# Performance work log

Measured on AMD Instinct MI355X. Metric: run time of the kernel, lower is better.

Reference implementation:

```python
import jax, jax.numpy as jnp
import numpy as np

N_NODES = 40000
N_EDGES = 640000
D = 128
N_GRAPHS = 64


def gcn_conv(x, W, b, edge_index):
    """PyG-style GCNConv: add self-loops, symmetric norm, linear, scatter-add."""
    n = x.shape[0]
    loops = jnp.arange(n, dtype=edge_index.dtype)
    src = jnp.concatenate([edge_index[0], loops])  # message sources (x_j)
    dst = jnp.concatenate([edge_index[1], loops])  # aggregation targets
    # deg computed over targets (col) with unit edge weights, incl. self-loops
    deg = jax.ops.segment_sum(jnp.ones_like(src, dtype=x.dtype), dst, num_segments=n)
    dinv = jnp.where(deg > 0, jax.lax.rsqrt(jnp.maximum(deg, 1.0)), 0.0)
    norm = dinv[src] * dinv[dst]  # [E+N]
    h = x @ W  # [N, d_out]
    out = jax.ops.segment_sum(norm[:, None] * h[src], dst, num_segments=n)
    return out + b


def global_mean_pool(x, batch, num_graphs):
    summed = jax.ops.segment_sum(x, batch, num_segments=num_graphs)
    counts = jax.ops.segment_sum(jnp.ones((x.shape[0],), x.dtype), batch, num_segments=num_graphs)
    return summed / jnp.maximum(counts, 1.0)[:, None]


def setup_inputs() -> dict:
    key = jax.random.key(0)
    ks = jax.random.split(key, 6)
    x = jax.random.normal(ks[0], (N_NODES, D), dtype=jnp.float32)
    edge_index = jax.random.randint(ks[1], (2, N_EDGES), 0, N_NODES)
    batch = jnp.sort(jax.random.randint(ks[2], (N_NODES,), 0, N_GRAPHS))
    s = 1.0 / np.sqrt(D)
    W1 = jax.random.normal(ks[3], (D, D), dtype=jnp.float32) * s
    W2 = jax.random.normal(ks[4], (D, D), dtype=jnp.float32) * s
    b1 = jnp.zeros((D,), jnp.float32)
    b2 = jnp.zeros((D,), jnp.float32)
    return {"x": x, "edge_index": edge_index, "batch": batch,
            "W1": W1, "b1": b1, "W2": W2, "b2": b2}


def reference(x, edge_index, batch, W1, b1, W2, b2):
    h = jax.nn.relu(gcn_conv(x, W1, b1, edge_index))
    h = gcn_conv(h, W2, b2, edge_index)  # no ReLU on last layer
    return global_mean_pool(h, batch, N_GRAPHS)
```

## Files before the change

### kernel.cpp

```cpp
#include <hip/hip_runtime.h>

#define D 128
#define N_GRAPHS 64

typedef unsigned int uint32;
typedef __attribute__((ext_vector_type(8))) _Float16 f16x8;
typedef __attribute__((ext_vector_type(4))) float f32x4;

__device__ __forceinline__ float hl(uint32 u) {
    return (float)__builtin_bit_cast(_Float16, (unsigned short)(u & 0xFFFF));
}
__device__ __forceinline__ float hh(uint32 u) {
    return (float)__builtin_bit_cast(_Float16, (unsigned short)(u >> 16));
}
__device__ __forceinline__ uint32 h2pair(float a, float b) {
    unsigned short ua = __builtin_bit_cast(unsigned short, (_Float16)a);
    unsigned short ub = __builtin_bit_cast(unsigned short, (_Float16)b);
    return (uint32)ua | ((uint32)ub << 16);
}

__global__ __launch_bounds__(256) void prep_kernel(int* __restrict__ cnt,
                                                   const float* __restrict__ W1,
                                                   uint32* __restrict__ Wh, int n) {
    int i = blockIdx.x * 256 + threadIdx.x;
    if (i < n) {
        cnt[i] = 0;
    } else if (i < n + D * (D / 2)) {
        int j = i - n;
        int nn = j & 127, kd = j >> 7;
        float v0 = W1[(size_t)(2 * kd) * D + nn];
        float v1 = W1[(size_t)(2 * kd + 1) * D + nn];
        Wh[nn * 64 + kd] = h2pair(v0, v1);
    }
}


__global__ void count_rank_kernel(const int* __restrict__ dst, int* __restrict__ cnt,
                                  int* __restrict__ rank, int E) {
    int e = blockIdx.x * blockDim.x + threadIdx.x;
    if (e < E) rank[e] = atomicAdd(&cnt[dst[e]], 1);
}

__global__ __launch_bounds__(1024) void scanA_kernel(const int* __restrict__ cnt,
                                                     int* __restrict__ rowptr,
                                                     int* __restrict__ tot,
                                                     float* __restrict__ dinv,
                                                     float* __restrict__ c,
                                                     const int* __restrict__ batch, int n) {
    __shared__ int swave[16];
    int t = threadIdx.x;
    int lane = t & 63, wave = t >> 6;
    int i = blockIdx.x * 1024 + t;
    {
        size_t f4base = (size_t)blockIdx.x * 1024 * 16;
        size_t f4lim = (size_t)n * 16;
        float4 z = make_float4(0.f, 0.f, 0.f, 0.f);
#pragma unroll
        for (int q = 0; q < 16; ++q) {
            size_t idx = f4base + (size_t)q * 1024 + t;
            if (idx < f4lim) ((float4*)c)[idx] = z;
        }
    }
    int orig = (i < n) ? cnt[i] : 0;
    int v = orig;
#pragma unroll
    for (int off = 1; off < 64; off <<= 1) {
        int u = __shfl_up(v, off, 64);
        if (lane >= off) v += u;
    }
    if (lane == 63) swave[wave] = v;
    __syncthreads();
    if (wave == 0) {
        int wv = (lane < 16) ? swave[lane] : 0;
#pragma unroll
        for (int off = 1; off < 16; off <<= 1) {
            int u = __shfl_up(wv, off, 64);
            if (lane >= off) wv += u;
        }
        if (lane < 16) swave[lane] = wv;
    }
    if (i < n) {
        float dv = rsqrtf((float)(orig + 1));
        dinv[i] = dv;
        c[(size_t)i * N_GRAPHS + batch[i]] = dv * dv;
    }
    __syncthreads();
    int incl = v + ((wave > 0) ? swave[wave - 1] : 0);
    if (i < n) rowptr[i] = incl - orig;
    if (t == 1023) tot[blockIdx.x] = incl;
}

__global__ __launch_bounds__(1024) void scanB_kernel(int* __restrict__ rowptr,
                                                     const int* __restrict__ tot,
                                                     int n, int nchunks) {
    __shared__ int soff;
    int b = blockIdx.x, t = threadIdx.x;
    if (t == 0) {
        int o = 0;
        for (int j = 0; j < b; ++j) o += tot[j];
        soff = o;
    }
    __syncthreads();
    int i = b * 1024 + t;
    if (i < n) rowptr[i] += soff;
    if (b == 0 && t == 0) {
        int o = 0;
        for (int j = 0; j < nchunks; ++j) o += tot[j];
        rowptr[n] = o;
    }
}


#define GBM 64

__global__ __launch_bounds__(256) void fill_gemm_kernel(
    const float* __restrict__ A, const uint32* __restrict__ Wh,
    uint32* __restrict__ hb, int M, int gemmBlocks,
    const int* __restrict__ src, const int* __restrict__ dst,
    const int* __restrict__ rowptr, const int* __restrict__ rank,
    int* __restrict__ col, const float* __restrict__ dinv,
    float* __restrict__ c, const int* __restrict__ batch, int E) {
    __shared__ uint32 lds[64 * 68];

    if (blockIdx.x >= gemmBlocks) {
        int e = (blockIdx.x - gemmBlocks) * 256 + threadIdx.x;
        if (e < E) {
            int s = src[e], d = dst[e];
            int pos = rowptr[d] + rank[e];
            col[pos] = s;
            float w = dinv[s] * dinv[d];
            atomicAdd(&c[(size_t)s * N_GRAPHS + batch[d]], w);
        }
        return;
    }

    uint32* As = lds;
    int tid = threadIdx.x;
    int row0 = blockIdx.x * GBM;

#pragma unroll
    for (int j = 0; j < 8; ++j) {
        int idx = tid + j * 256;
        int r = idx >> 5, c4 = idx & 31;
        float4 v = make_float4(0.f, 0.f, 0.f, 0.f);
        if (row0 + r < M) v = *(const float4*)&A[(size_t)(row0 + r) * D + c4 * 4];
        As[r * 68 + c4 * 2 + 0] = h2pair(v.x, v.y);
        As[r * 68 + c4 * 2 + 1] = h2pair(v.z, v.w);
    }
    __syncthreads();

    int wave = tid >> 6, lane = tid & 63;
    int quad = lane >> 4, l16 = lane & 15;
    int wr = (wave & 1) * 32;
    int wc = (wave >> 1) * 64;
    f32x4 acc[2][4];
#pragma unroll
    for (int mi = 0; mi < 2; ++mi)
#pragma unroll
        for (int ni = 0; ni < 4; ++ni) acc[mi][ni] = (f32x4){0.f, 0.f, 0.f, 0.f};

#pragma unroll
    for (int ks = 0; ks < 4; ++ks) {
        int kd = ks * 16 + quad * 4;
        f16x8 a0 = *(f16x8*)&As[(wr + l16) * 68 + kd];
        f16x8 a1 = *(f16x8*)&As[(wr + 16 + l16) * 68 + kd];
        f16x8 b0 = *(const f16x8*)&Wh[(wc + l16) * 64 + kd];
        f16x8 b1 = *(const f16x8*)&Wh[(wc + 16 + l16) * 64 + kd];
        f16x8 b2 = *(const f16x8*)&Wh[(wc + 32 + l16) * 64 + kd];
        f16x8 b3 = *(const f16x8*)&Wh[(wc + 48 + l16) * 64 + kd];
        acc[0][0] = __builtin_amdgcn_mfma_f32_16x16x32_f16(a0, b0, acc[0][0], 0, 0, 0);
        acc[0][1] = __builtin_amdgcn_mfma_f32_16x16x32_f16(a0, b1, acc[0][1], 0, 0, 0);
        acc[0][2] = __builtin_amdgcn_mfma_f32_16x16x32_f16(a0, b2, acc[0][2], 0, 0, 0);
        acc[0][3] = __builtin_amdgcn_mfma_f32_16x16x32_f16(a0, b3, acc[0][3], 0, 0, 0);
        acc[1][0] = __builtin_amdgcn_mfma_f32_16x16x32_f16(a1, b0, acc[1][0], 0, 0, 0);
        acc[1][1] = __builtin_amdgcn_mfma_f32_16x16x32_f16(a1, b1, acc[1][1], 0, 0, 0);
        acc[1][2] = __builtin_amdgcn_mfma_f32_16x16x32_f16(a1, b2, acc[1][2], 0, 0, 0);
        acc[1][3] = __builtin_amdgcn_mfma_f32_16x16x32_f16(a1, b3, acc[1][3], 0, 0, 0);
    }
    __syncthreads();

    unsigned short* cs = (unsigned short*)lds;
#pragma unroll
    for (int mi = 0; mi < 2; ++mi)
#pragma unroll
        for (int ni = 0; ni < 4; ++ni)
#pragma unroll
            for (int r = 0; r < 4; ++r) {
                int row = wr + mi * 16 + quad * 4 + r;
                int col2 = wc + ni * 16 + l16;
                cs[row * 128 + col2] =
                    __builtin_bit_cast(unsigned short, (_Float16)acc[mi][ni][r]);
            }
    __syncthreads();
#pragma unroll
    for (int j = 0; j < 4; ++j) {
        int idx = tid + j * 256;
        int r = idx >> 4, q = idx & 15;
        if (row0 + r < M)
            *(uint4*)&hb[(size_t)(row0 + r) * 64 + q * 4] = *(uint4*)&lds[r * 64 + q * 4];
    }
}


__global__ __launch_bounds__(128) void agg_kernel(const uint32* __restrict__ hb,
                                                  const int* __restrict__ rowptr,
                                                  const int* __restrict__ col,
                                                  const float* __restrict__ dinv,
                                                  const float* __restrict__ bias,
                                                  uint32* __restrict__ h1, int n) {
    int tid = threadIdx.x;
    int lane32 = tid & 31;
    int slot = tid >> 5;
    int node = blockIdx.x * 4 + slot;
    if (node >= n) return;
    const uint2* __restrict__ h2 = (const uint2*)hb;

    float di = dinv[node];
    float ws = di * di;
    uint2 su = h2[(size_t)node * 32 + lane32];
    float a0 = ws * hl(su.x), a1 = ws * hh(su.x);
    float a2 = ws * hl(su.y), a3 = ws * hh(su.y);

    int k = rowptr[node], end = rowptr[node + 1];
    for (; k + 8 <= end; k += 8) {
        uint2 v[8];
        float w[8];
#pragma unroll
        for (int j = 0; j < 8; ++j) {
            int s = col[k + j];
            w[j] = dinv[s] * di;
            v[j] = h2[(size_t)s * 32 + lane32];
        }
#pragma unroll
        for (int j = 0; j < 8; ++j) {
            a0 = fmaf(w[j], hl(v[j].x), a0);
            a1 = fmaf(w[j], hh(v[j].x), a1);
            a2 = fmaf(w[j], hl(v[j].y), a2);
            a3 = fmaf(w[j], hh(v[j].y), a3);
        }
    }
    for (; k < end; ++k) {
        int s = col[k];
        float w = dinv[s] * di;
        uint2 v = h2[(size_t)s * 32 + lane32];
        a0 = fmaf(w, hl(v.x), a0);
        a1 = fmaf(w, hh(v.x), a1);
        a2 = fmaf(w, hl(v.y), a2);
        a3 = fmaf(w, hh(v.y), a3);
    }

    float4 b4 = ((const float4*)bias)[lane32];
    a0 = fmaxf(a0 + b4.x, 0.f);
    a1 = fmaxf(a1 + b4.y, 0.f);
    a2 = fmaxf(a2 + b4.z, 0.f);
    a3 = fmaxf(a3 + b4.w, 0.f);
    uint2 o;
    o.x = h2pair(a0, a1);
    o.y = h2pair(a2, a3);
    ((uint2*)h1)[(size_t)node * 32 + lane32] = o;
}


#define GP_NB 256
#define GP_T 16

__global__ __launch_bounds__(256) void gp_kernel(const float* __restrict__ c,
                                                 const uint32* __restrict__ H1,
                                                 float* __restrict__ Ppart, int n) {
    __shared__ float sc[GP_T][N_GRAPHS];
    __shared__ uint32 sh[GP_T][64];
    int t = threadIdx.x;
    int b = blockIdx.x;
    int jpb = (n + GP_NB - 1) / GP_NB;
    int j0 = b * jpb;
    int j1 = min(j0 + jpb, n);
    int g0 = (t & 7) * 8;
    int f0 = (t >> 3) * 4;
    float acc[8][4];
#pragma unroll
    for (int a = 0; a < 8; ++a)
#pragma unroll
        for (int q = 0; q < 4; ++q) acc[a][q] = 0.f;

    for (int jt = j0; jt < j1; jt += GP_T) {
        int cnt = min(GP_T, j1 - jt);
        {
            int r = t >> 4, q = t & 15;
            float4 v = (r < cnt) ? *(const float4*)&c[(size_t)(jt + r) * N_GRAPHS + q * 4]
                                 : make_float4(0.f, 0.f, 0.f, 0.f);
            *(float4*)&sc[r][q * 4] = v;
        }
        {
            int r = t >> 4, q = t & 15;
            uint4 v = make_uint4(0, 0, 0, 0);
            if (r < cnt) v = *(const uint4*)&H1[(size_t)(jt + r) * 64 + q * 4];
            *(uint4*)&sh[r][q * 4] = v;
        }
        __syncthreads();
#pragma unroll
        for (int r = 0; r < GP_T; ++r) {
            float cw[8], hv[4];
            *(float4*)&cw[0] = *(float4*)&sc[r][g0];
            *(float4*)&cw[4] = *(float4*)&sc[r][g0 + 4];
            uint32 u0 = sh[r][f0 >> 1], u1 = sh[r][(f0 >> 1) + 1];
            hv[0] = hl(u0); hv[1] = hh(u0); hv[2] = hl(u1); hv[3] = hh(u1);
#pragma unroll
            for (int a = 0; a < 8; ++a)
#pragma unroll
                for (int q = 0; q < 4; ++q) acc[a][q] = fmaf(cw[a], hv[q], acc[a][q]);
        }
        __syncthreads();
    }
    float* P = &Ppart[(size_t)b * N_GRAPHS * D];
#pragma unroll
    for (int a = 0; a < 8; ++a)
        *(float4*)&P[(size_t)(g0 + a) * D + f0] =
            make_float4(acc[a][0], acc[a][1], acc[a][2], acc[a][3]);
}

__global__ __launch_bounds__(256) void out_kernel(const float* __restrict__ Ppart,
                                                  const float* __restrict__ W2,
                                                  const float* __restrict__ b2,
                                                  const int* __restrict__ batch, int n,
                                                  float* __restrict__ out) {
    __shared__ float gs[D];
    __shared__ float part[2][D];
    __shared__ float srinv;
    int g = blockIdx.x, t = threadIdx.x;
    int f = t & 127, half = t >> 7;
    if (t == 0) {
        int lo = 0, hi = n;
        while (lo < hi) { int mid = (lo + hi) >> 1; if (batch[mid] < g) lo = mid + 1; else hi = mid; }
        int lb = lo;
        int g1 = g + 1;
        lo = 0; hi = n;
        while (lo < hi) { int mid = (lo + hi) >> 1; if (batch[mid] < g1) lo = mid + 1; else hi = mid; }
        int cg = lo - lb;
        srinv = (cg > 0) ? 1.0f / (float)cg : 0.0f;
    }
    float s = 0.f;
    int b0 = half * (GP_NB / 2);
#pragma unroll 8
    for (int b = b0; b < b0 + GP_NB / 2; ++b)
        s += Ppart[((size_t)b * N_GRAPHS + g) * D + f];
    part[half][f] = s;
    __syncthreads();
    if (half == 0) gs[f] = part[0][f] + part[1][f];
    __syncthreads();
    float acc = 0.f;
    int k0 = half * (D / 2);
#pragma unroll 8
    for (int k = k0; k < k0 + D / 2; ++k) acc = fmaf(gs[k], W2[k * D + f], acc);
    part[half][f] = acc;
    __syncthreads();
    if (half == 0) {
        float a = part[0][f] + part[1][f];
        float r = srinv;
        out[g * D + f] = (r > 0.f) ? fmaf(a, r, b2[f]) : 0.f;
    }
}


extern "C" void kernel_launch(void* const* d_in, const int* in_sizes, int n_in,
                              void* d_out, int out_size, void* d_ws, size_t ws_size,
                              hipStream_t stream) {
    const float* x  = (const float*)d_in[0];
    const int*   ei = (const int*)d_in[1];
    const int*   batch = (const int*)d_in[2];
    const float* W1 = (const float*)d_in[3];
    const float* b1 = (const float*)d_in[4];
    const float* W2 = (const float*)d_in[5];
    const float* b2 = (const float*)d_in[6];
    float* out = (float*)d_out;

    const int n = in_sizes[2];
    const int E = in_sizes[1] / 2;
    const int* src = ei;
    const int* dst = ei + E;

    char* ws = (char*)d_ws;
    size_t off = 0;
    auto carve = [&](size_t bytes) {
        size_t o = off;
        off = (off + bytes + 255) & ~(size_t)255;
        return (void*)(ws + o);
    };
    int*    cnt    = (int*)carve((size_t)n * 4);
    int*    rowptr = (int*)carve((size_t)(n + 1) * 4);
    float*  dinv   = (float*)carve((size_t)n * 4);
    int*    col    = (int*)carve((size_t)E * 4);
    uint32* hb     = (uint32*)carve((size_t)n * D * 2);
    uint32* h1     = (uint32*)carve((size_t)n * D * 2);
    float*  c      = (float*)carve((size_t)n * N_GRAPHS * 4);
    int*    tot    = (int*)carve(64 * 4);
    int*    rank   = (int*)carve((size_t)E * 4);
    uint32* Wh     = (uint32*)carve((size_t)D * (D / 2) * 4);
    float*  Ppart  = (float*)hb;
    (void)ws_size;

    const int nchunks = (n + 1023) >> 10;

    prep_kernel<<<(n + D * (D / 2) + 255) / 256, 256, 0, stream>>>(cnt, W1, Wh, n);

    count_rank_kernel<<<(E + 255) / 256, 256, 0, stream>>>(dst, cnt, rank, E);
    scanA_kernel<<<nchunks, 1024, 0, stream>>>(cnt, rowptr, tot, dinv, c, batch, n);
    scanB_kernel<<<nchunks, 1024, 0, stream>>>(rowptr, tot, n, nchunks);

    const int gemmBlocks = (n + GBM - 1) / GBM;
    const int fillBlocks = (E + 255) / 256;
    fill_gemm_kernel<<<gemmBlocks + fillBlocks, 256, 0, stream>>>(
        x, Wh, hb, n, gemmBlocks, src, dst, rowptr, rank, col, dinv, c, batch, E);

    agg_kernel<<<(n + 3) / 4, 128, 0, stream>>>(hb, rowptr, col, dinv, b1, h1, n);

    gp_kernel<<<GP_NB, 256, 0, stream>>>(c, h1, Ppart, n);
    out_kernel<<<N_GRAPHS, 256, 0, stream>>>(Ppart, W2, b2, batch, n, out);
}
```

Measured before the change: 220.8 us.

## Co-schedule GEMM with edge counting and fold pooling-weight atomics into aggregation

Moves the edge-degree counting (atomic rank assignment) into the GEMM launch so it overlaps with the matrix multiply, instead of pairing the GEMM with the CSR fill. The fill becomes a separate lightweight kernel after the scan, and the per-edge scatter of normalized weights into the pooling coefficient matrix c moves into the aggregation kernel, where one lane per edge issues the atomic. This changes the cross-stage schedule and adds a kernel launch, and it puts extra atomics on the critical aggregation path in exchange for removing the random dinv/batch gathers from the fill stage.

```diff
diff --git a/kernel.cpp b/kernel.cpp
--- a/kernel.cpp
+++ b/kernel.cpp
@@ -35,102 +35,18 @@
 }
 
 
-__global__ void count_rank_kernel(const int* __restrict__ dst, int* __restrict__ cnt,
-                                  int* __restrict__ rank, int E) {
-    int e = blockIdx.x * blockDim.x + threadIdx.x;
-    if (e < E) rank[e] = atomicAdd(&cnt[dst[e]], 1);
-}
-
-__global__ __launch_bounds__(1024) void scanA_kernel(const int* __restrict__ cnt,
-                                                     int* __restrict__ rowptr,
-                                                     int* __restrict__ tot,
-                                                     float* __restrict__ dinv,
-                                                     float* __restrict__ c,
-                                                     const int* __restrict__ batch, int n) {
-    __shared__ int swave[16];
-    int t = threadIdx.x;
-    int lane = t & 63, wave = t >> 6;
-    int i = blockIdx.x * 1024 + t;
-    {
-        size_t f4base = (size_t)blockIdx.x * 1024 * 16;
-        size_t f4lim = (size_t)n * 16;
-        float4 z = make_float4(0.f, 0.f, 0.f, 0.f);
-#pragma unroll
-        for (int q = 0; q < 16; ++q) {
-            size_t idx = f4base + (size_t)q * 1024 + t;
-            if (idx < f4lim) ((float4*)c)[idx] = z;
-        }
-    }
-    int orig = (i < n) ? cnt[i] : 0;
-    int v = orig;
-#pragma unroll
-    for (int off = 1; off < 64; off <<= 1) {
-        int u = __shfl_up(v, off, 64);
-        if (lane >= off) v += u;
-    }
-    if (lane == 63) swave[wave] = v;
-    __syncthreads();
-    if (wave == 0) {
-        int wv = (lane < 16) ? swave[lane] : 0;
-#pragma unroll
-        for (int off = 1; off < 16; off <<= 1) {
-            int u = __shfl_up(wv, off, 64);
-            if (lane >= off) wv += u;
-        }
-        if (lane < 16) swave[lane] = wv;
-    }
-    if (i < n) {
-        float dv = rsqrtf((float)(orig + 1));
-        dinv[i] = dv;
-        c[(size_t)i * N_GRAPHS + batch[i]] = dv * dv;
-    }
-    __syncthreads();
-    int incl = v + ((wave > 0) ? swave[wave - 1] : 0);
-    if (i < n) rowptr[i] = incl - orig;
-    if (t == 1023) tot[blockIdx.x] = incl;
-}
-
-__global__ __launch_bounds__(1024) void scanB_kernel(int* __restrict__ rowptr,
-                                                     const int* __restrict__ tot,
-                                                     int n, int nchunks) {
-    __shared__ int soff;
-    int b = blockIdx.x, t = threadIdx.x;
-    if (t == 0) {
-        int o = 0;
-        for (int j = 0; j < b; ++j) o += tot[j];
-        soff = o;
-    }
-    __syncthreads();
-    int i = b * 1024 + t;
-    if (i < n) rowptr[i] += soff;
-    if (b == 0 && t == 0) {
-        int o = 0;
-        for (int j = 0; j < nchunks; ++j) o += tot[j];
-        rowptr[n] = o;
-    }
-}
-
-
 #define GBM 64
 
-__global__ __launch_bounds__(256) void fill_gemm_kernel(
+__global__ __launch_bounds__(256) void count_gemm_kernel(
     const float* __restrict__ A, const uint32* __restrict__ Wh,
     uint32* __restrict__ hb, int M, int gemmBlocks,
-    const int* __restrict__ src, const int* __restrict__ dst,
-    const int* __restrict__ rowptr, const int* __restrict__ rank,
-    int* __restrict__ col, const float* __restrict__ dinv,
-    float* __restrict__ c, const int* __restrict__ batch, int E) {
+    const int* __restrict__ dst, int* __restrict__ cnt,
+    int* __restrict__ rank, int E) {
     __shared__ uint32 lds[64 * 68];
 
     if (blockIdx.x >= gemmBlocks) {
         int e = (blockIdx.x - gemmBlocks) * 256 + threadIdx.x;
-        if (e < E) {
-            int s = src[e], d = dst[e];
-            int pos = rowptr[d] + rank[e];
-            col[pos] = s;
-            float w = dinv[s] * dinv[d];
-            atomicAdd(&c[(size_t)s * N_GRAPHS + batch[d]], w);
-        }
+        if (e < E) rank[e] = atomicAdd(&cnt[dst[e]], 1);
         return;
     }
 
@@ -202,11 +118,90 @@
 }
 
 
+__global__ __launch_bounds__(1024) void scanA_kernel(const int* __restrict__ cnt,
+                                                     int* __restrict__ rowptr,
+                                                     int* __restrict__ tot,
+                                                     float* __restrict__ dinv,
+                                                     float* __restrict__ c,
+                                                     const int* __restrict__ batch, int n) {
+    __shared__ int swave[16];
+    int t = threadIdx.x;
+    int lane = t & 63, wave = t >> 6;
+    int i = blockIdx.x * 1024 + t;
+    {
+        size_t f4base = (size_t)blockIdx.x * 1024 * 16;
+        size_t f4lim = (size_t)n * 16;
+        float4 z = make_float4(0.f, 0.f, 0.f, 0.f);
+#pragma unroll
+        for (int q = 0; q < 16; ++q) {
+            size_t idx = f4base + (size_t)q * 1024 + t;
+            if (idx < f4lim) ((float4*)c)[idx] = z;
+        }
+    }
+    int orig = (i < n) ? cnt[i] : 0;
+    int v = orig;
+#pragma unroll
+    for (int off = 1; off < 64; off <<= 1) {
+        int u = __shfl_up(v, off, 64);
+        if (lane >= off) v += u;
+    }
+    if (lane == 63) swave[wave] = v;
+    __syncthreads();
+    if (wave == 0) {
+        int wv = (lane < 16) ? swave[lane] : 0;
+#pragma unroll
+        for (int off = 1; off < 16; off <<= 1) {
+            int u = __shfl_up(wv, off, 64);
+            if (lane >= off) wv += u;
+        }
+        if (lane < 16) swave[lane] = wv;
+    }
+    if (i < n) {
+        float dv = rsqrtf((float)(orig + 1));
+        dinv[i] = dv;
+        c[(size_t)i * N_GRAPHS + batch[i]] = dv * dv;
+    }
+    __syncthreads();
+    int incl = v + ((wave > 0) ? swave[wave - 1] : 0);
+    if (i < n) rowptr[i] = incl - orig;
+    if (t == 1023) tot[blockIdx.x] = incl;
+}
+
+__global__ __launch_bounds__(1024) void scanB_kernel(int* __restrict__ rowptr,
+                                                     const int* __restrict__ tot,
+                                                     int n, int nchunks) {
+    __shared__ int soff;
+    int b = blockIdx.x, t = threadIdx.x;
+    if (t == 0) {
+        int o = 0;
+        for (int j = 0; j < b; ++j) o += tot[j];
+        soff = o;
+    }
+    __syncthreads();
+    int i = b * 1024 + t;
+    if (i < n) rowptr[i] += soff;
+    if (b == 0 && t == 0) {
+        int o = 0;
+        for (int j = 0; j < nchunks; ++j) o += tot[j];
+        rowptr[n] = o;
+    }
+}
+
+__global__ void fill_kernel(const int* __restrict__ src, const int* __restrict__ dst,
+                            const int* __restrict__ rowptr, const int* __restrict__ rank,
+                            int* __restrict__ col, int E) {
+    int e = blockIdx.x * blockDim.x + threadIdx.x;
+    if (e < E) col[rowptr[dst[e]] + rank[e]] = src[e];
+}
+
+
 __global__ __launch_bounds__(128) void agg_kernel(const uint32* __restrict__ hb,
                                                   const int* __restrict__ rowptr,
                                                   const int* __restrict__ col,
                                                   const float* __restrict__ dinv,
                                                   const float* __restrict__ bias,
+                                                  const int* __restrict__ batch,
+                                                  float* __restrict__ c,
                                                   uint32* __restrict__ h1, int n) {
     int tid = threadIdx.x;
     int lane32 = tid & 31;
@@ -216,6 +211,7 @@
     const uint2* __restrict__ h2 = (const uint2*)hb;
 
     float di = dinv[node];
+    int bg = batch[node];
     float ws = di * di;
     uint2 su = h2[(size_t)node * 32 + lane32];
     float a0 = ws * hl(su.x), a1 = ws * hh(su.x);
@@ -230,6 +226,7 @@
             int s = col[k + j];
             w[j] = dinv[s] * di;
             v[j] = h2[(size_t)s * 32 + lane32];
+            if (lane32 == j) atomicAdd(&c[(size_t)s * N_GRAPHS + bg], w[j]);
         }
 #pragma unroll
         for (int j = 0; j < 8; ++j) {
@@ -243,6 +240,7 @@
         int s = col[k];
         float w = dinv[s] * di;
         uint2 v = h2[(size_t)s * 32 + lane32];
+        if (lane32 == 0) atomicAdd(&c[(size_t)s * N_GRAPHS + bg], w);
         a0 = fmaf(w, hl(v.x), a0);
         a1 = fmaf(w, hh(v.x), a1);
         a2 = fmaf(w, hl(v.y), a2);
@@ -402,16 +400,16 @@
 
     prep_kernel<<<(n + D * (D / 2) + 255) / 256, 256, 0, stream>>>(cnt, W1, Wh, n);
 
-    count_rank_kernel<<<(E + 255) / 256, 256, 0, stream>>>(dst, cnt, rank, E);
+    const int gemmBlocks = (n + GBM - 1) / GBM;
+    const int countBlocks = (E + 255) / 256;
+    count_gemm_kernel<<<gemmBlocks + countBlocks, 256, 0, stream>>>(
+        x, Wh, hb, n, gemmBlocks, dst, cnt, rank, E);
+
     scanA_kernel<<<nchunks, 1024, 0, stream>>>(cnt, rowptr, tot, dinv, c, batch, n);
     scanB_kernel<<<nchunks, 1024, 0, stream>>>(rowptr, tot, n, nchunks);
-
-    const int gemmBlocks = (n + GBM - 1) / GBM;
-    const int fillBlocks = (E + 255) / 256;
-    fill_gemm_kernel<<<gemmBlocks + fillBlocks, 256, 0, stream>>>(
-        x, Wh, hb, n, gemmBlocks, src, dst, rowptr, rank, col, dinv, c, batch, E);
-
-    agg_kernel<<<(n + 3) / 4, 128, 0, stream>>>(hb, rowptr, col, dinv, b1, h1, n);
+    fill_kernel<<<(E + 255) / 256, 256, 0, stream>>>(src, dst, rowptr, rank, col, E);
+
+    agg_kernel<<<(n + 3) / 4, 128, 0, stream>>>(hb, rowptr, col, dinv, b1, batch, c, h1, n);
 
     gp_kernel<<<GP_NB, 256, 0, stream>>>(c, h1, Ppart, n);
     out_kernel<<<N_GRAPHS, 256, 0, stream>>>(Ppart, W2, b2, batch, n, out);
```

Result: slower. 228.9 us (+3.7%).
